# Performance work log

Hardware: AMD Instinct MI355X
Metric: run time of the kernel (lower is better)

The kernel has to match this reference:

```python
import jax, jax.numpy as jnp
import numpy as np

GRID = (32, 32)          # 448 // 14
IMG = (448, 448)
SIGMA = 4.0              # anomalib AnomalyMapGenerator default smoothing


def _l2norm(x, axis=-1, eps=1e-12):
    return x / jnp.clip(jnp.linalg.norm(x, axis=axis, keepdims=True), eps, None)


def _gaussian_blur(x, sigma=SIGMA):
    # kornia-style: kernel_size = 2*int(4*sigma+0.5)+1, reflect padding, separable conv
    radius = int(4.0 * sigma + 0.5)
    t = jnp.arange(-radius, radius + 1, dtype=x.dtype)
    k = jnp.exp(-0.5 * (t / sigma) ** 2)
    k = k / k.sum()
    xp = jnp.pad(x, ((0, 0), (0, 0), (radius, radius), (radius, radius)), mode='reflect')
    kh = k.reshape(1, 1, -1, 1)
    kw = k.reshape(1, 1, 1, -1)
    dn = ('NCHW', 'OIHW', 'NCHW')
    y = jax.lax.conv_general_dilated(xp, kh, (1, 1), 'VALID', dimension_numbers=dn)
    return jax.lax.conv_general_dilated(y, kw, (1, 1), 'VALID', dimension_numbers=dn)


def setup_inputs() -> dict:
    key = jax.random.key(0)
    k1, k2 = jax.random.split(key)
    features = jax.random.normal(k1, (8, 1024, 384), dtype=jnp.float32)
    memory_bank = jax.random.normal(k2, (65536, 384), dtype=jnp.float32)
    return {"features": features, "memory_bank": memory_bank}


def reference(features, memory_bank):
    # features: (B, N, D) patch tokens from DINOv2; memory_bank: (M, D)
    b, n, _ = features.shape
    f = _l2norm(features)                 # F.normalize(features, p=2, dim=1) on flattened patches
    mb = _l2norm(memory_bank)             # bank stores normalized embeddings
    sim = jnp.einsum('bnd,md->bnm', f, mb)            # (B, N, M) cosine similarity
    dists = jnp.clip(1.0 - sim, 0.0, 2.0)
    min_dists = dists.min(axis=2)                     # k = num_neighbours = 1 -> row min
    num_top = max(int(n * 0.01), 1)
    top_vals = jax.lax.top_k(min_dists, num_top)[0]
    pred_score = top_vals.mean(axis=1, keepdims=True) # (B, 1)
    amap = min_dists.reshape(b, 1, *GRID)
    amap = jax.image.resize(amap, (b, 1, *IMG), method='bilinear')
    anomaly_map = _gaussian_blur(amap)                # (B, 1, H, W)
    return pred_score, anomaly_map
```

## Files before the change

kernel.cpp:

```cpp
#include <hip/hip_runtime.h>
#include <hip/hip_bf16.h>

#define NROW_F 8192
#define NROW_B 65536
#define KDIM   384
#define BM 128
#define BN 128
#define NSUB 16
#define NGRP (NROW_B / (BN * NSUB))
#define NBM  (NROW_F / BM)
#define NWG  (NBM * NGRP)

#define LDSA 0
#define LDSB 49152
#define LDSS 73728
#define LDSR 49152
#define LDS_TOT 81920

typedef int   i32x4 __attribute__((ext_vector_type(4)));
typedef float f32x4 __attribute__((ext_vector_type(4)));

static __device__ __forceinline__ void stage16(const void* g, void* l) {
  __builtin_amdgcn_global_load_lds(
      (const __attribute__((address_space(1))) unsigned int*)g,
      (__attribute__((address_space(3))) unsigned int*)l, 16, 0, 0);
}

__global__ __launch_bounds__(256) void quantize_rows_kernel(
    const float* __restrict__ in, char* __restrict__ out8,
    float* __restrict__ scales, int nrows) {
  int row = blockIdx.x * 8 + (threadIdx.x >> 5);
  int l   = threadIdx.x & 31;
  if (row >= nrows) return;
  const f32x4* r = (const f32x4*)(in + (size_t)row * KDIM);
  f32x4 v[3];
  float ss = 0.f, mx = 0.f;
#pragma unroll
  for (int i = 0; i < 3; ++i) {
    v[i] = r[l + i * 32];
#pragma unroll
    for (int j = 0; j < 4; ++j) {
      ss += v[i][j] * v[i][j];
      mx = fmaxf(mx, fabsf(v[i][j]));
    }
  }
#pragma unroll
  for (int d = 1; d < 32; d <<= 1) {
    ss += __shfl_xor(ss, d, 64);
    mx = fmaxf(mx, __shfl_xor(mx, d, 64));
  }
  mx = fmaxf(mx, 1e-30f);
  float inv = rsqrtf(fmaxf(ss, 1e-24f));
  float scl = 127.0f / mx;
  if (l == 0) scales[row] = mx * inv * (1.0f / 127.0f);
  char* o = out8 + (size_t)row * KDIM;
#pragma unroll
  for (int i = 0; i < 3; ++i) {
    char4 c;
    c.x = (char)__float2int_rn(v[i][0] * scl);
    c.y = (char)__float2int_rn(v[i][1] * scl);
    c.z = (char)__float2int_rn(v[i][2] * scl);
    c.w = (char)__float2int_rn(v[i][3] * scl);
    *(char4*)(o + (l + i * 32) * 4) = c;
  }
}

__global__ __launch_bounds__(256, 2) void maxsim_kernel(
    const char* __restrict__ F8,
    const char* __restrict__ B8,
    const float* __restrict__ sA,
    const float* __restrict__ sB,
    float* __restrict__ partial) {
  __shared__ __align__(16) char smem[LDS_TOT];

  const int tid  = threadIdx.x;
  const int wv   = tid >> 6;
  const int lane = tid & 63;
  const int l15  = lane & 15;
  const int lhi  = lane >> 4;
  const int wr   = wv >> 1;
  const int wc   = wv & 1;

  const int wg  = (blockIdx.x & 7) * (NWG / 8) + (blockIdx.x >> 3);
  const int bm  = wg & (NBM - 1);
  const int grp = wg >> 6;
  const size_t brow = (size_t)bm * BM;

  const int srow = tid >> 2;
  const int gsw  = (tid & 3) ^ ((tid >> 3) & 3);

  {
    const char* gA = F8 + (size_t)(brow + srow) * KDIM + gsw * 16;
    char* lA = smem + LDSA + wv * 1024;
#pragma unroll
    for (int kt = 0; kt < 6; ++kt) {
      stage16(gA + kt * 64,             lA + kt * 8192);
      stage16(gA + kt * 64 + 64 * KDIM, lA + kt * 8192 + 4096);
    }
  }
  {
    const char* gs = (const char*)(sB + (size_t)grp * 2048) + tid * 16;
    stage16(gs,        smem + LDSS + wv * 1024);
    stage16(gs + 4096, smem + LDSS + 4096 + wv * 1024);
  }

  auto stageB = [&](int s2, int koff, int buf) {
    const char* g = B8 + ((size_t)grp * 2048 + s2 * 128 + srow) * KDIM
                    + koff * 64 + gsw * 16;
    char* l = smem + LDSB + buf * 8192 + wv * 1024;
    stage16(g, l);
    stage16(g + (size_t)64 * KDIM, l + 4096);
  };
  stageB(0, 0, 0);
  stageB(0, 1, 1);
  stageB(0, 2, 2);

  const int cof = ((l15 >> 1) & 3) << 4;

  auto ldA8 = [&](int k6, int m) -> i32x4 {
    int byte = k6 * 8192 + (wr * 64 + m * 16 + l15) * 64 + ((lhi << 4) ^ cof);
    return *reinterpret_cast<const i32x4*>(smem + LDSA + byte);
  };
  auto ldB8 = [&](int buf, int n) -> i32x4 {
    int byte = buf * 8192 + (wc * 64 + n * 16 + l15) * 64 + ((lhi << 4) ^ cof);
    return *reinterpret_cast<const i32x4*>(smem + LDSB + byte);
  };

  i32x4 acc[4][4];
  f32x4 vm[4];
#pragma unroll
  for (int m = 0; m < 4; ++m) {
    vm[m] = f32x4{-1e30f, -1e30f, -1e30f, -1e30f};
#pragma unroll
    for (int n = 0; n < 4; ++n) acc[m][n] = i32x4{0, 0, 0, 0};
  }

  asm volatile("s_waitcnt vmcnt(4)" ::: "memory");
  __builtin_amdgcn_s_barrier();

  i32x4 a[6][4];
#pragma unroll
  for (int k6 = 0; k6 < 6; ++k6)
#pragma unroll
    for (int m = 0; m < 4; ++m) a[k6][m] = ldA8(k6, m);

  i32x4 bA[4], bB[4];
#pragma unroll
  for (int n = 0; n < 4; ++n) bA[n] = ldB8(0, n);
  asm volatile("s_waitcnt lgkmcnt(0)" ::: "memory");

#define PHASE(K6, BC, BN_) do {                                               \
    asm volatile("s_waitcnt vmcnt(2)" ::: "memory");                          \
    __builtin_amdgcn_s_barrier();                                             \
    __builtin_amdgcn_sched_barrier(0);                                        \
    _Pragma("unroll")                                                         \
    for (int n = 0; n < 4; ++n) BN_[n] = ldB8(((K6) + 1) % 3, n);             \
    {                                                                         \
      const int s2 = ((K6) < 3) ? sub : ((sub + 1) & (NSUB - 1));             \
      stageB(s2, ((K6) + 3) % 6, (K6) % 3);                                   \
    }                                                                         \
    __builtin_amdgcn_sched_barrier(0);                                        \
    __builtin_amdgcn_s_setprio(1);                                            \
    _Pragma("unroll")                                                         \
    for (int n = 0; n < 4; ++n)                                               \
      _Pragma("unroll")                                                       \
      for (int m = 0; m < 4; ++m)                                             \
        acc[m][n] = __builtin_amdgcn_mfma_i32_16x16x64_i8(                    \
            a[K6][m], BC[n], acc[m][n], 0, 0, 0);                             \
    __builtin_amdgcn_s_setprio(0);                                            \
    asm volatile("s_waitcnt lgkmcnt(0)" ::: "memory");                        \
    __builtin_amdgcn_sched_barrier(0);                                        \
  } while (0)

  for (int sub = 0; sub < NSUB; ++sub) {
    PHASE(0, bA, bB);
    PHASE(1, bB, bA);
    PHASE(2, bA, bB);
    PHASE(3, bB, bA);
    PHASE(4, bA, bB);
    PHASE(5, bB, bA);
    float sb[4];
#pragma unroll
    for (int n = 0; n < 4; ++n)
      sb[n] = *reinterpret_cast<const float*>(
          smem + LDSS + (sub * 128 + wc * 64 + n * 16 + l15) * 4);
#pragma unroll
    for (int m = 0; m < 4; ++m) {
#pragma unroll
      for (int n = 0; n < 4; ++n)
#pragma unroll
        for (int j = 0; j < 4; ++j)
          vm[m][j] = fmaxf(vm[m][j], (float)acc[m][n][j] * sb[n]);
#pragma unroll
      for (int n = 0; n < 4; ++n) acc[m][n] = i32x4{0, 0, 0, 0};
    }
  }
#undef PHASE

  asm volatile("s_waitcnt vmcnt(0)" ::: "memory");
#pragma unroll
  for (int d = 1; d < 16; d <<= 1)
#pragma unroll
    for (int m = 0; m < 4; ++m)
#pragma unroll
      for (int j = 0; j < 4; ++j)
        vm[m][j] = fmaxf(vm[m][j], __shfl_xor(vm[m][j], d, 64));

  float* red = (float*)(smem + LDSR);
  __syncthreads();
  if (l15 == 0) {
#pragma unroll
    for (int m = 0; m < 4; ++m)
#pragma unroll
      for (int j = 0; j < 4; ++j)
        red[wc * 128 + wr * 64 + m * 16 + lhi * 4 + j] = vm[m][j];
  }
  __syncthreads();
  if (tid < BM) {
    float x = fmaxf(red[tid], red[128 + tid]);
    partial[(size_t)grp * NROW_F + brow + tid] = x * sA[brow + tid];
  }
}

__global__ __launch_bounds__(256) void combw_kernel(
    const float* __restrict__ partial, float* __restrict__ md,
    float* __restrict__ W) {
  if (blockIdx.x < 32) {
    int r = blockIdx.x * 256 + threadIdx.x;
    float m = -1e30f;
#pragma unroll
    for (int c = 0; c < NGRP; ++c) m = fmaxf(m, partial[(size_t)c * NROW_F + r]);
    float d = 1.0f - m;
    md[r] = fminf(fmaxf(d, 0.0f), 2.0f);
    return;
  }
  int idx = (blockIdx.x - 32) * 256 + threadIdx.x;
  int y = idx >> 5, g = idx & 31;
  float ksum = 0.f, acc = 0.f;
#pragma unroll
  for (int t = -16; t <= 16; ++t) {
    float ft = (float)t * 0.25f;
    float kv = expf(-0.5f * ft * ft);
    ksum += kv;
    int p = y + t;
    p = (p < 0) ? -p : ((p > 447) ? 894 - p : p);
    float src = ((float)p + 0.5f) * (1.0f / 14.0f) - 0.5f;
    float fl = floorf(src);
    int i0 = (int)fl;
    float fr = src - fl;
    int c0 = i0 < 0 ? 0 : (i0 > 31 ? 31 : i0);
    int i1 = i0 + 1;
    int c1 = i1 < 0 ? 0 : (i1 > 31 ? 31 : i1);
    float w = 0.f;
    if (c0 == g) w += 1.0f - fr;
    if (c1 == g) w += fr;
    acc += kv * w;
  }
  W[idx] = acc / ksum;
}

__global__ __launch_bounds__(64) void topk_kernel(
    const float* __restrict__ partial, float* __restrict__ out) {
  int b = blockIdx.x, lane = threadIdx.x;
  float vals[16];
#pragma unroll
  for (int k = 0; k < 16; ++k) {
    int r = b * 1024 + k * 64 + lane;
    float m = -1e30f;
#pragma unroll
    for (int c = 0; c < NGRP; ++c) m = fmaxf(m, partial[(size_t)c * NROW_F + r]);
    float d = 1.0f - m;
    vals[k] = fminf(fmaxf(d, 0.0f), 2.0f);
  }
  float total = 0.f;
  for (int it = 0; it < 10; ++it) {
    float lb = vals[0]; int li = 0;
#pragma unroll
    for (int k = 1; k < 16; ++k)
      if (vals[k] > lb) { lb = vals[k]; li = k; }
    float wm = lb;
#pragma unroll
    for (int d = 1; d < 64; d <<= 1) wm = fmaxf(wm, __shfl_xor(wm, d, 64));
    unsigned long long mask = __ballot(lb == wm);
    int winner = (int)(__ffsll((unsigned long long)mask) - 1);
    bool kill = (lane == winner);
#pragma unroll
    for (int k = 0; k < 16; ++k)
      vals[k] = (kill && k == li) ? -1e30f : vals[k];
    total += wm;
  }
  if (lane == 0) out[b] = total * 0.1f;
}

__global__ __launch_bounds__(256) void map_kernel(
    const float* __restrict__ md, const float* __restrict__ W,
    float* __restrict__ out) {
  __shared__ float tmpv[32];
  int y = blockIdx.x % 448;
  int b = blockIdx.x / 448;
  int tid = threadIdx.x;
  if (tid < 32) {
    const float* w = W + y * 32;
    const float* m = md + b * 1024 + tid;
    float s = 0.f;
#pragma unroll
    for (int gy = 0; gy < 32; ++gy) s += w[gy] * m[gy * 32];
    tmpv[tid] = s;
  }
  __syncthreads();
  for (int x = tid; x < 448; x += 256) {
    const float* w = W + x * 32;
    float s = 0.f;
#pragma unroll
    for (int gx = 0; gx < 32; ++gx) s += w[gx] * tmpv[gx];
    out[(size_t)blockIdx.x * 448 + x] = s;
  }
}

extern "C" void kernel_launch(void* const* d_in, const int* in_sizes, int n_in,
                              void* d_out, int out_size, void* d_ws, size_t ws_size,
                              hipStream_t stream) {
  const float* features = (const float*)d_in[0];
  const float* bank     = (const float*)d_in[1];
  float* out = (float*)d_out;

  char* ws = (char*)d_ws;
  char*  mb8     = ws;
  char*  f8      = ws + 25165824;
  float* sB      = (float*)(ws + 28311552);
  float* sA      = (float*)(ws + 28573696);
  float* partial = (float*)(ws + 28606464);
  float* md      = (float*)(ws + 29655040);
  float* W       = (float*)(ws + 29687808);

  quantize_rows_kernel<<<NROW_B / 8, 256, 0, stream>>>(bank, mb8, sB, NROW_B);
  quantize_rows_kernel<<<NROW_F / 8, 256, 0, stream>>>(features, f8, sA, NROW_F);
  maxsim_kernel<<<NWG, 256, 0, stream>>>(f8, mb8, sA, sB, partial);
  combw_kernel<<<88, 256, 0, stream>>>(partial, md, W);
  topk_kernel<<<8, 64, 0, stream>>>(partial, out);
  map_kernel<<<8 * 448, 256, 0, stream>>>(md, W, out + 8);
}
```

Before: 240.2 us.

## Deepen B staging pipeline to four LDS buffers and merge small kernels

The maxsim kernel now loads the whole A tile into registers first and reuses the freed A LDS region for the scale and reduction buffers. That frees room for a fourth B buffer, so B prefetch runs one stage further ahead, and the sub-tile loop is unrolled by two to keep buffer indices static. The two quantize launches are merged into one grid, and the combine and top-k kernels are merged into one launch, cutting launch overhead. The trade-offs are an extra barrier and a full vmcnt(0) wait before the A register loads, plus more code from the unroll.

```diff
diff --git a/kernel.cpp b/kernel.cpp
--- a/kernel.cpp
+++ b/kernel.cpp
@@ -12,9 +12,9 @@
 #define NWG  (NBM * NGRP)
 
 #define LDSA 0
+#define LDSS2 0
+#define LDSR2 16384
 #define LDSB 49152
-#define LDSS 73728
-#define LDSR 49152
 #define LDS_TOT 81920
 
 typedef int   i32x4 __attribute__((ext_vector_type(4)));
@@ -26,12 +26,18 @@
       (__attribute__((address_space(3))) unsigned int*)l, 16, 0, 0);
 }
 
-__global__ __launch_bounds__(256) void quantize_rows_kernel(
-    const float* __restrict__ in, char* __restrict__ out8,
-    float* __restrict__ scales, int nrows) {
-  int row = blockIdx.x * 8 + (threadIdx.x >> 5);
-  int l   = threadIdx.x & 31;
-  if (row >= nrows) return;
+__global__ __launch_bounds__(256) void quantize_all_kernel(
+    const float* __restrict__ bank, char* __restrict__ mb8, float* __restrict__ sB,
+    const float* __restrict__ feat, char* __restrict__ f8, float* __restrict__ sA) {
+  const float* in; char* out8; float* scales; int row;
+  if (blockIdx.x < NROW_B / 8) {
+    in = bank; out8 = mb8; scales = sB;
+    row = blockIdx.x * 8 + (threadIdx.x >> 5);
+  } else {
+    in = feat; out8 = f8; scales = sA;
+    row = (blockIdx.x - NROW_B / 8) * 8 + (threadIdx.x >> 5);
+  }
+  int l = threadIdx.x & 31;
   const f32x4* r = (const f32x4*)(in + (size_t)row * KDIM);
   f32x4 v[3];
   float ss = 0.f, mx = 0.f;
@@ -98,12 +104,27 @@
       stage16(gA + kt * 64 + 64 * KDIM, lA + kt * 8192 + 4096);
     }
   }
+  asm volatile("s_waitcnt vmcnt(0)" ::: "memory");
+  __builtin_amdgcn_s_barrier();
+
+  const int cof = ((l15 >> 1) & 3) << 4;
+  auto ldA8 = [&](int k6, int m) -> i32x4 {
+    int byte = k6 * 8192 + (wr * 64 + m * 16 + l15) * 64 + ((lhi << 4) ^ cof);
+    return *reinterpret_cast<const i32x4*>(smem + LDSA + byte);
+  };
+  i32x4 a[6][4];
+#pragma unroll
+  for (int k6 = 0; k6 < 6; ++k6)
+#pragma unroll
+    for (int m = 0; m < 4; ++m) a[k6][m] = ldA8(k6, m);
+  asm volatile("s_waitcnt lgkmcnt(0)" ::: "memory");
+  __builtin_amdgcn_s_barrier();
+
   {
     const char* gs = (const char*)(sB + (size_t)grp * 2048) + tid * 16;
-    stage16(gs,        smem + LDSS + wv * 1024);
-    stage16(gs + 4096, smem + LDSS + 4096 + wv * 1024);
-  }
-
+    stage16(gs,        smem + LDSS2 + wv * 1024);
+    stage16(gs + 4096, smem + LDSS2 + 4096 + wv * 1024);
+  }
   auto stageB = [&](int s2, int koff, int buf) {
     const char* g = B8 + ((size_t)grp * 2048 + s2 * 128 + srow) * KDIM
                     + koff * 64 + gsw * 16;
@@ -114,13 +135,8 @@
   stageB(0, 0, 0);
   stageB(0, 1, 1);
   stageB(0, 2, 2);
-
-  const int cof = ((l15 >> 1) & 3) << 4;
-
-  auto ldA8 = [&](int k6, int m) -> i32x4 {
-    int byte = k6 * 8192 + (wr * 64 + m * 16 + l15) * 64 + ((lhi << 4) ^ cof);
-    return *reinterpret_cast<const i32x4*>(smem + LDSA + byte);
-  };
+  stageB(0, 3, 3);
+
   auto ldB8 = [&](int buf, int n) -> i32x4 {
     int byte = buf * 8192 + (wc * 64 + n * 16 + l15) * 64 + ((lhi << 4) ^ cof);
     return *reinterpret_cast<const i32x4*>(smem + LDSB + byte);
@@ -135,30 +151,22 @@
     for (int n = 0; n < 4; ++n) acc[m][n] = i32x4{0, 0, 0, 0};
   }
 
-  asm volatile("s_waitcnt vmcnt(4)" ::: "memory");
+  asm volatile("s_waitcnt vmcnt(6)" ::: "memory");
   __builtin_amdgcn_s_barrier();
-
-  i32x4 a[6][4];
-#pragma unroll
-  for (int k6 = 0; k6 < 6; ++k6)
-#pragma unroll
-    for (int m = 0; m < 4; ++m) a[k6][m] = ldA8(k6, m);
 
   i32x4 bA[4], bB[4];
 #pragma unroll
   for (int n = 0; n < 4; ++n) bA[n] = ldB8(0, n);
   asm volatile("s_waitcnt lgkmcnt(0)" ::: "memory");
 
-#define PHASE(K6, BC, BN_) do {                                               \
-    asm volatile("s_waitcnt vmcnt(2)" ::: "memory");                          \
+#define PHASE(K6, SUBX, RB, SBUF, BC, BN_) do {                               \
+    asm volatile("s_waitcnt vmcnt(4)" ::: "memory");       \
     __builtin_amdgcn_s_barrier();                                             \
     __builtin_amdgcn_sched_barrier(0);                                        \
     _Pragma("unroll")                                                         \
-    for (int n = 0; n < 4; ++n) BN_[n] = ldB8(((K6) + 1) % 3, n);             \
-    {                                                                         \
-      const int s2 = ((K6) < 3) ? sub : ((sub + 1) & (NSUB - 1));             \
-      stageB(s2, ((K6) + 3) % 6, (K6) % 3);                                   \
-    }                                                                         \
+    for (int n = 0; n < 4; ++n) BN_[n] = ldB8(RB, n);                         \
+    stageB(((K6) < 2) ? (SUBX) : (((SUBX) + 1) & (NSUB - 1)),                 \
+           ((K6) + 4) % 6, SBUF);                                             \
     __builtin_amdgcn_sched_barrier(0);                                        \
     __builtin_amdgcn_s_setprio(1);                                            \
     _Pragma("unroll")                                                         \
@@ -172,30 +180,42 @@
     __builtin_amdgcn_sched_barrier(0);                                        \
   } while (0)
 
-  for (int sub = 0; sub < NSUB; ++sub) {
-    PHASE(0, bA, bB);
-    PHASE(1, bB, bA);
-    PHASE(2, bA, bB);
-    PHASE(3, bB, bA);
-    PHASE(4, bA, bB);
-    PHASE(5, bB, bA);
-    float sb[4];
-#pragma unroll
-    for (int n = 0; n < 4; ++n)
-      sb[n] = *reinterpret_cast<const float*>(
-          smem + LDSS + (sub * 128 + wc * 64 + n * 16 + l15) * 4);
-#pragma unroll
-    for (int m = 0; m < 4; ++m) {
-#pragma unroll
-      for (int n = 0; n < 4; ++n)
-#pragma unroll
-        for (int j = 0; j < 4; ++j)
-          vm[m][j] = fmaxf(vm[m][j], (float)acc[m][n][j] * sb[n]);
-#pragma unroll
-      for (int n = 0; n < 4; ++n) acc[m][n] = i32x4{0, 0, 0, 0};
-    }
+#define FOLD(S) do {                                                          \
+    float sb[4];                                                              \
+    _Pragma("unroll")                                                         \
+    for (int n = 0; n < 4; ++n)                                               \
+      sb[n] = *reinterpret_cast<const float*>(                                \
+          smem + LDSS2 + ((S) * 128 + wc * 64 + n * 16 + l15) * 4);           \
+    _Pragma("unroll")                                                         \
+    for (int m = 0; m < 4; ++m) {                                             \
+      _Pragma("unroll")                                                       \
+      for (int n = 0; n < 4; ++n)                                             \
+        _Pragma("unroll")                                                     \
+        for (int j = 0; j < 4; ++j)                                           \
+          vm[m][j] = fmaxf(vm[m][j], (float)acc[m][n][j] * sb[n]);            \
+      _Pragma("unroll")                                                       \
+      for (int n = 0; n < 4; ++n) acc[m][n] = i32x4{0, 0, 0, 0};              \
+    }                                                                         \
+  } while (0)
+
+  for (int sub = 0; sub < NSUB; sub += 2) {
+    PHASE(0, sub, 1, 0, bA, bB);
+    PHASE(1, sub, 2, 1, bB, bA);
+    PHASE(2, sub, 3, 2, bA, bB);
+    PHASE(3, sub, 0, 3, bB, bA);
+    PHASE(4, sub, 1, 0, bA, bB);
+    PHASE(5, sub, 2, 1, bB, bA);
+    FOLD(sub);
+    PHASE(0, sub + 1, 3, 2, bA, bB);
+    PHASE(1, sub + 1, 0, 3, bB, bA);
+    PHASE(2, sub + 1, 1, 0, bA, bB);
+    PHASE(3, sub + 1, 2, 1, bB, bA);
+    PHASE(4, sub + 1, 3, 2, bA, bB);
+    PHASE(5, sub + 1, 0, 3, bB, bA);
+    FOLD(sub + 1);
   }
 #undef PHASE
+#undef FOLD
 
   asm volatile("s_waitcnt vmcnt(0)" ::: "memory");
 #pragma unroll
@@ -206,7 +226,7 @@
       for (int j = 0; j < 4; ++j)
         vm[m][j] = fmaxf(vm[m][j], __shfl_xor(vm[m][j], d, 64));
 
-  float* red = (float*)(smem + LDSR);
+  float* red = (float*)(smem + LDSR2);
   __syncthreads();
   if (l15 == 0) {
 #pragma unroll
@@ -222,9 +242,9 @@
   }
 }
 
-__global__ __launch_bounds__(256) void combw_kernel(
+__global__ __launch_bounds__(256) void combw_topk_kernel(
     const float* __restrict__ partial, float* __restrict__ md,
-    float* __restrict__ W) {
+    float* __restrict__ W, float* __restrict__ out) {
   if (blockIdx.x < 32) {
     int r = blockIdx.x * 256 + threadIdx.x;
     float m = -1e30f;
@@ -234,34 +254,34 @@
     md[r] = fminf(fmaxf(d, 0.0f), 2.0f);
     return;
   }
-  int idx = (blockIdx.x - 32) * 256 + threadIdx.x;
-  int y = idx >> 5, g = idx & 31;
-  float ksum = 0.f, acc = 0.f;
-#pragma unroll
-  for (int t = -16; t <= 16; ++t) {
-    float ft = (float)t * 0.25f;
-    float kv = expf(-0.5f * ft * ft);
-    ksum += kv;
-    int p = y + t;
-    p = (p < 0) ? -p : ((p > 447) ? 894 - p : p);
-    float src = ((float)p + 0.5f) * (1.0f / 14.0f) - 0.5f;
-    float fl = floorf(src);
-    int i0 = (int)fl;
-    float fr = src - fl;
-    int c0 = i0 < 0 ? 0 : (i0 > 31 ? 31 : i0);
-    int i1 = i0 + 1;
-    int c1 = i1 < 0 ? 0 : (i1 > 31 ? 31 : i1);
-    float w = 0.f;
-    if (c0 == g) w += 1.0f - fr;
-    if (c1 == g) w += fr;
-    acc += kv * w;
-  }
-  W[idx] = acc / ksum;
-}
-
-__global__ __launch_bounds__(64) void topk_kernel(
-    const float* __restrict__ partial, float* __restrict__ out) {
-  int b = blockIdx.x, lane = threadIdx.x;
+  if (blockIdx.x < 88) {
+    int idx = (blockIdx.x - 32) * 256 + threadIdx.x;
+    int y = idx >> 5, g = idx & 31;
+    float ksum = 0.f, acc = 0.f;
+#pragma unroll
+    for (int t = -16; t <= 16; ++t) {
+      float ft = (float)t * 0.25f;
+      float kv = expf(-0.5f * ft * ft);
+      ksum += kv;
+      int p = y + t;
+      p = (p < 0) ? -p : ((p > 447) ? 894 - p : p);
+      float src = ((float)p + 0.5f) * (1.0f / 14.0f) - 0.5f;
+      float fl = floorf(src);
+      int i0 = (int)fl;
+      float fr = src - fl;
+      int c0 = i0 < 0 ? 0 : (i0 > 31 ? 31 : i0);
+      int i1 = i0 + 1;
+      int c1 = i1 < 0 ? 0 : (i1 > 31 ? 31 : i1);
+      float w = 0.f;
+      if (c0 == g) w += 1.0f - fr;
+      if (c1 == g) w += fr;
+      acc += kv * w;
+    }
+    W[idx] = acc / ksum;
+    return;
+  }
+  if (threadIdx.x >= 64) return;
+  int b = blockIdx.x - 88, lane = threadIdx.x;
   float vals[16];
 #pragma unroll
   for (int k = 0; k < 16; ++k) {
@@ -282,7 +302,7 @@
 #pragma unroll
     for (int d = 1; d < 64; d <<= 1) wm = fmaxf(wm, __shfl_xor(wm, d, 64));
     unsigned long long mask = __ballot(lb == wm);
-    int winner = (int)(__ffsll((unsigned long long)mask) - 1);
+    int winner = (int)(__ffsll(mask) - 1);
     bool kill = (lane == winner);
 #pragma unroll
     for (int k = 0; k < 16; ++k)
@@ -333,10 +353,9 @@
   float* md      = (float*)(ws + 29655040);
   float* W       = (float*)(ws + 29687808);
 
-  quantize_rows_kernel<<<NROW_B / 8, 256, 0, stream>>>(bank, mb8, sB, NROW_B);
-  quantize_rows_kernel<<<NROW_F / 8, 256, 0, stream>>>(features, f8, sA, NROW_F);
+  quantize_all_kernel<<<(NROW_B + NROW_F) / 8, 256, 0, stream>>>(
+      bank, mb8, sB, features, f8, sA);
   maxsim_kernel<<<NWG, 256, 0, stream>>>(f8, mb8, sA, sB, partial);
-  combw_kernel<<<88, 256, 0, stream>>>(partial, md, W);
-  topk_kernel<<<8, 64, 0, stream>>>(partial, out);
+  combw_topk_kernel<<<96, 256, 0, stream>>>(partial, md, W, out);
   map_kernel<<<8 * 448, 256, 0, stream>>>(md, W, out + 8);
 }
```

After: 284.3 us. +18.4%, slower.
